# Performance work log

Hardware: AMD Instinct MI355X
Metric: run time of the kernel (lower is better)

Reference implementation:

```python
import jax, jax.numpy as jnp
import numpy as np

N, IN_DIM, HID, HEADS, OUT = 4096, 512, 256, 2, 40
LN_EPS = 1e-5


def setup_inputs() -> dict:
    key = jax.random.key(0)
    ks = jax.random.split(key, 12)
    s_in = 1.0 / np.sqrt(IN_DIM)
    s_o = 1.0 / np.sqrt(2 * HID)
    adj = jax.random.randint(ks[0], (HEADS, N, N), 0, 2).astype(jnp.float32)
    h = jax.random.normal(ks[1], (N, IN_DIM), dtype=jnp.float32)
    Wq = jax.random.uniform(ks[2], (HEADS, IN_DIM, HID), minval=-s_in, maxval=s_in)
    bq = jax.random.uniform(ks[3], (HEADS, HID), minval=-s_in, maxval=s_in)
    Wk = jax.random.uniform(ks[4], (HEADS, IN_DIM, HID), minval=-s_in, maxval=s_in)
    bk = jax.random.uniform(ks[5], (HEADS, HID), minval=-s_in, maxval=s_in)
    Wv = jax.random.uniform(ks[6], (HEADS, IN_DIM, HID), minval=-s_in, maxval=s_in)
    bv = jax.random.uniform(ks[7], (HEADS, HID), minval=-s_in, maxval=s_in)
    Wo = jax.random.uniform(ks[8], (2 * HID, IN_DIM), minval=-s_o, maxval=s_o)
    bo = jax.random.uniform(ks[9], (IN_DIM,), minval=-s_o, maxval=s_o)
    gamma = jnp.ones((IN_DIM,), jnp.float32)
    beta = jnp.zeros((IN_DIM,), jnp.float32)
    Wp = jax.random.uniform(ks[10], (IN_DIM, OUT), minval=-s_in, maxval=s_in)
    bp = jax.random.uniform(ks[11], (OUT,), minval=-s_in, maxval=s_in)
    return dict(adj=adj, h=h, Wq=Wq, bq=bq, Wk=Wk, bk=bk, Wv=Wv, bv=bv,
                Wo=Wo, bo=bo, gamma=gamma, beta=beta, Wp=Wp, bp=bp)


def reference(adj, h, Wq, bq, Wk, bk, Wv, bv, Wo, bo, gamma, beta, Wp, bp):
    # Per-head projections, vectorized over the head axis. [H, N, D]
    Q = jnp.einsum('ni,hid->hnd', h, Wq) + bq[:, None, :]
    K = jnp.einsum('ni,hid->hnd', h, Wk) + bk[:, None, :]
    V = jnp.einsum('ni,hid->hnd', h, Wv) + bv[:, None, :]
    # Dense QK^T, elementwise-multiplied (not -inf masked) by per-head adjacency.
    scores = jnp.einsum('hnd,hmd->hnm', Q, K) * adj          # [H, N, N]
    attn = jax.nn.softmax(scores, axis=-1)
    X = jnp.einsum('hnm,hmd->hnd', attn, V)                  # [H, N, D]
    # cat([X0, X1], dim=1) -> [N, H*D]
    X_final = jnp.transpose(X, (1, 0, 2)).reshape(N, HEADS * HID)
    z = X_final @ Wo + bo                                    # [N, IN_DIM]
    mu = jnp.mean(z, axis=-1, keepdims=True)
    var = jnp.var(z, axis=-1, keepdims=True)
    M = (z - mu) * jax.lax.rsqrt(var + LN_EPS) * gamma + beta
    return jax.nn.softmax(M @ Wp + bp, axis=1)               # [N, OUT]
```

## Files before the change

kernel.cpp:

```cpp
#include <hip/hip_runtime.h>
#include <hip/hip_bf16.h>

#define N_TOK 4096
#define D_IN  512
#define D_HID 256
#define N_OUT 40

typedef _Float16 half8 __attribute__((ext_vector_type(8)));
typedef _Float16 half4 __attribute__((ext_vector_type(4)));
typedef float    f32x4 __attribute__((ext_vector_type(4)));

__device__ __forceinline__ void async_copy16(const _Float16* g, _Float16* l) {
  __builtin_amdgcn_global_load_lds(
      (const __attribute__((address_space(1))) unsigned int*)(g),
      (__attribute__((address_space(3))) unsigned int*)(l), 16, 0, 0);
}

__device__ __forceinline__ void transpose_tile(const float* __restrict__ src, int in_ncols,
                                               _Float16* __restrict__ dst, int out_ncols,
                                               int i0, int d0, float* lds )
{
  int tid = threadIdx.x;
  int l15 = tid & 15, l4 = tid >> 4;
#pragma unroll
  for (int p = 0; p < 4; p++) {
    int ii = p * 16 + l4;
    float4 x = *(const float4*)(src + (size_t)(i0 + ii) * in_ncols + d0 + l15 * 4);
    lds[(l15 * 4 + 0) * 65 + ii] = x.x;
    lds[(l15 * 4 + 1) * 65 + ii] = x.y;
    lds[(l15 * 4 + 2) * 65 + ii] = x.z;
    lds[(l15 * 4 + 3) * 65 + ii] = x.w;
  }
  __syncthreads();
  int dd = tid >> 2, chunk = tid & 3;
  half8 o0, o1;
#pragma unroll
  for (int j = 0; j < 8; j++) o0[j] = (_Float16)lds[dd * 65 + chunk * 16 + j];
#pragma unroll
  for (int j = 0; j < 8; j++) o1[j] = (_Float16)lds[dd * 65 + chunk * 16 + 8 + j];
  *(half8*)(dst + (size_t)(d0 + dd) * out_ncols + i0 + chunk * 16) = o0;
  *(half8*)(dst + (size_t)(d0 + dd) * out_ncols + i0 + chunk * 16 + 8) = o1;
}

__global__ void prep_kernel(const float* __restrict__ h, const float* __restrict__ Wq,
                            const float* __restrict__ Wk, const float* __restrict__ Wv,
                            const float* __restrict__ Wo, const float* __restrict__ Wp,
                            _Float16* __restrict__ h16, _Float16* __restrict__ Wqt,
                            _Float16* __restrict__ Wkt, _Float16* __restrict__ Wvt,
                            _Float16* __restrict__ Wot, _Float16* __restrict__ Wpt)
{
  __shared__ float lds[64 * 65];
  int b = blockIdx.x, tid = threadIdx.x;
  if (b < 1024) {
    int base = b * 2048 + tid * 8;
    float4 x0 = *(const float4*)(h + base);
    float4 x1 = *(const float4*)(h + base + 4);
    half8 o;
    o[0]=(_Float16)x0.x; o[1]=(_Float16)x0.y; o[2]=(_Float16)x0.z; o[3]=(_Float16)x0.w;
    o[4]=(_Float16)x1.x; o[5]=(_Float16)x1.y; o[6]=(_Float16)x1.z; o[7]=(_Float16)x1.w;
    *(half8*)(h16 + base) = o;
  } else if (b < 1216) {
    int t = b - 1024;
    int mat = t >> 5;
    int m = mat >> 1, head = mat & 1;
    const float* W = (m==0 ? Wq : (m==1 ? Wk : Wv)) + head * (D_IN * D_HID);
    _Float16* Wt   = (m==0 ? Wqt : (m==1 ? Wkt : Wvt)) + head * (D_IN * D_HID);
    int tt = t & 31;
    int i0 = (tt >> 2) * 64, d0 = (tt & 3) * 64;
    transpose_tile(W, D_HID, Wt, D_IN, i0, d0, lds);
  } else if (b < 1280) {
    int t = b - 1216;
    int i0 = (t >> 3) * 64, d0 = (t & 7) * 64;
    transpose_tile(Wo, D_IN, Wot, D_IN, i0, d0, lds);
  } else {
    int blk = b - 1280;
    int idx = blk * 1024 + tid * 4;
    int j = idx >> 9, i = idx & 511;
    half4 o;
#pragma unroll
    for (int u = 0; u < 4; u++)
      o[u] = (j < N_OUT) ? (_Float16)Wp[(i + u) * N_OUT + j] : (_Float16)0.f;
    *(half4*)(Wpt + j * D_IN + i) = o;
  }
}

__global__ __launch_bounds__(256, 2) void proj_kernel(
    const _Float16* __restrict__ h16, const _Float16* __restrict__ W6 ,
    const _Float16* __restrict__ Wvt,
    const float* __restrict__ bq, const float* __restrict__ bk,
    const float* __restrict__ bv,
    _Float16* __restrict__ Q16, _Float16* __restrict__ K16,
    _Float16* __restrict__ VT16)
{
  __shared__ __align__(16) _Float16 Atile[128 * 64];
  __shared__ __align__(16) _Float16 Btile[128 * 64];

  int b = blockIdx.x;
  int tid = threadIdx.x, w = tid >> 6, lane = tid & 63, quad = lane >> 4, cL = lane & 15;
  int wr = w >> 1, wc = w & 1;

  const _Float16 *Asrc, *Bsrc;
  int isV;
  int m0 = 0, n0 = 0, head = 0, mh = 0;
  if (b < 256) {
    isV = 0;
    m0 = (b >> 3) * 128;
    int ct = b & 7;
    mh = ct >> 1;
    n0 = (ct & 1) * 128;
    Asrc = h16 + (size_t)m0 * D_IN;
    Bsrc = W6 + (size_t)(ct * 128) * D_IN;
  } else {
    isV = 1;
    int t = b - 256;
    head = t >> 6;
    int tt = t & 63;
    m0 = (tt >> 5) * 128;
    n0 = (tt & 31) * 128;
    Asrc = Wvt + (size_t)head * (D_HID * D_IN) + (size_t)m0 * D_IN;
    Bsrc = h16 + (size_t)n0 * D_IN;
  }

  const f32x4 z4 = {0.f, 0.f, 0.f, 0.f};
  f32x4 acc[4][4];
#pragma unroll
  for (int i = 0; i < 4; i++)
#pragma unroll
    for (int j = 0; j < 4; j++) acc[i][j] = z4;

  int r8 = lane >> 3, chs = (lane & 7) ^ r8;

  for (int kc = 0; kc < 8; kc++) {
    __syncthreads();
#pragma unroll
    for (int g = 0; g < 4; g++) {
      int row = (w * 4 + g) * 8 + r8;
      async_copy16(Asrc + (size_t)row * D_IN + kc * 64 + chs * 8, Atile + (w * 4 + g) * 512);
      async_copy16(Bsrc + (size_t)row * D_IN + kc * 64 + chs * 8, Btile + (w * 4 + g) * 512);
    }
    __syncthreads();
#pragma unroll
    for (int kk = 0; kk < 2; kk++) {
      int ch = ((kk * 4 + quad) ^ (cL & 7)) * 8;
      half8 a[4], bf[4];
#pragma unroll
      for (int mt = 0; mt < 4; mt++)
        a[mt] = *(const half8*)(Atile + (wr * 64 + mt * 16 + cL) * 64 + ch);
#pragma unroll
      for (int nt = 0; nt < 4; nt++)
        bf[nt] = *(const half8*)(Btile + (wc * 64 + nt * 16 + cL) * 64 + ch);
#pragma unroll
      for (int mt = 0; mt < 4; mt++)
#pragma unroll
        for (int nt = 0; nt < 4; nt++)
          acc[mt][nt] = __builtin_amdgcn_mfma_f32_16x16x32_f16(a[mt], bf[nt], acc[mt][nt], 0, 0, 0);
    }
  }

  if (!isV) {
    _Float16* Out = (mh < 2 ? Q16 + (size_t)mh * (N_TOK * D_HID)
                            : K16 + (size_t)(mh - 2) * (N_TOK * D_HID));
    const float* bias = (mh < 2 ? bq + mh * D_HID : bk + (mh - 2) * D_HID);
#pragma unroll
    for (int mt = 0; mt < 4; mt++) {
      int row = m0 + wr * 64 + mt * 16 + quad * 4;
#pragma unroll
      for (int nt = 0; nt < 4; nt++) {
        int colg = n0 + wc * 64 + nt * 16 + cL;
        float bb = bias[colg];
#pragma unroll
        for (int reg = 0; reg < 4; reg++)
          Out[(size_t)(row + reg) * D_HID + colg] = (_Float16)(acc[mt][nt][reg] + bb);
      }
    }
  } else {
    _Float16* VTh = VT16 + (size_t)head * (N_TOK * D_HID);
    const float* bvh = bv + head * D_HID;
#pragma unroll
    for (int mt = 0; mt < 4; mt++) {
      int d0r = m0 + wr * 64 + mt * 16 + quad * 4;
      float bvv[4];
#pragma unroll
      for (int reg = 0; reg < 4; reg++) bvv[reg] = bvh[d0r + reg];
#pragma unroll
      for (int nt = 0; nt < 4; nt++) {
        int tok = n0 + wc * 64 + nt * 16 + cL;
#pragma unroll
        for (int reg = 0; reg < 4; reg++)
          VTh[(size_t)(d0r + reg) * N_TOK + tok] = (_Float16)(acc[mt][nt][reg] + bvv[reg]);
      }
    }
  }
}

__global__ __launch_bounds__(256, 2) void attn_kernel(
    const float* __restrict__ adj, const _Float16* __restrict__ Q16,
    const _Float16* __restrict__ K16, const _Float16* __restrict__ VT16,
    _Float16* __restrict__ Opart, float* __restrict__ Mpart, float* __restrict__ Lpart)
{
  __shared__ __align__(16) _Float16 Ktile[64 * 256];
  __shared__ __align__(16) _Float16 VTtile[256 * 64];
  __shared__ __align__(16) _Float16 Pbuf[4 * 16 * 72];

  int b = blockIdx.x;
  int head = (b >> 2) & 1;
  int gs = b & 3;
  int q0 = (b >> 3) * 64;

  int tid = threadIdx.x;
  int w = tid >> 6, lane = tid & 63, quad = lane >> 4, cL = lane & 15;

  const _Float16* Qh = Q16 + head * (N_TOK * D_HID);
  const _Float16* Kh = K16 + head * (N_TOK * D_HID);
  const _Float16* Vh = VT16 + head * (N_TOK * D_HID);
  const float* adjh = adj + (size_t)head * N_TOK * N_TOK;

  int qrow = q0 + w * 16;
  int nstart = gs * 1024;
  const f32x4 z4 = {0.f, 0.f, 0.f, 0.f};

  half8 qf[8];
#pragma unroll
  for (int t = 0; t < 8; t++)
    qf[t] = *(const half8*)(Qh + (qrow + cL) * D_HID + t * 32 + quad * 8);

  f32x4 acc[16];
#pragma unroll
  for (int i = 0; i < 16; i++) acc[i] = z4;
  float m_i[4] = {-1e30f, -1e30f, -1e30f, -1e30f};
  float l_i[4] = {0.f, 0.f, 0.f, 0.f};

  _Float16* pb = Pbuf + w * (16 * 72);

  const float* adjR[4];
#pragma unroll
  for (int reg = 0; reg < 4; reg++)
    adjR[reg] = adjh + (size_t)(qrow + quad * 4 + reg) * N_TOK + nstart + cL;

  int l5 = lane >> 5, l31 = lane & 31;
  int l3 = lane >> 3, l7 = lane & 7;

  for (int it = 0; it < 16; ++it) {
    int n0 = nstart + it * 64;

    __syncthreads();

#pragma unroll
    for (int i = 0; i < 8; i++) {
      int g = w * 8 + i;
      int rK = 2 * g + l5;
      int cK = l31 ^ (rK & 7);
      async_copy16(Kh + (size_t)(n0 + rK) * D_HID + cK * 8, Ktile + g * 512);
      int rV = g * 8 + l3;
      int cV = l7 ^ (rV & 7);
      async_copy16(Vh + (size_t)rV * N_TOK + n0 + cV * 8, VTtile + g * 512);
    }
    float av[4][4];
#pragma unroll
    for (int reg = 0; reg < 4; reg++)
#pragma unroll
      for (int ct = 0; ct < 4; ct++)
        av[reg][ct] = __builtin_nontemporal_load(adjR[reg] + it * 64 + ct * 16);

    __syncthreads();

    f32x4 s[4];
#pragma unroll
    for (int ct = 0; ct < 4; ct++) s[ct] = z4;
#pragma unroll
    for (int t = 0; t < 8; t++) {
#pragma unroll
      for (int ct = 0; ct < 4; ct++) {
        int rK = ct * 16 + cL;
        int ck = (t * 4 + quad) ^ (rK & 7);
        half8 kf = *(const half8*)(Ktile + rK * 256 + ck * 8);
        s[ct] = __builtin_amdgcn_mfma_f32_16x16x32_f16(qf[t], kf, s[ct], 0, 0, 0);
      }
    }

    float alpha[4];
#pragma unroll
    for (int reg = 0; reg < 4; reg++) {
#pragma unroll
      for (int ct = 0; ct < 4; ct++) s[ct][reg] *= av[reg][ct];
      float mx = fmaxf(fmaxf(s[0][reg], s[1][reg]), fmaxf(s[2][reg], s[3][reg]));
#pragma unroll
      for (int msk = 1; msk < 16; msk <<= 1) mx = fmaxf(mx, __shfl_xor(mx, msk, 16));
      float mnew = fmaxf(m_i[reg], mx);
      alpha[reg] = __expf(m_i[reg] - mnew);
      m_i[reg] = mnew;
      float rs = 0.f;
#pragma unroll
      for (int ct = 0; ct < 4; ct++) {
        float p = __expf(s[ct][reg] - mnew);
        s[ct][reg] = p;
        rs += p;
      }
#pragma unroll
      for (int msk = 1; msk < 16; msk <<= 1) rs += __shfl_xor(rs, msk, 16);
      l_i[reg] = l_i[reg] * alpha[reg] + rs;
    }

#pragma unroll
    for (int reg = 0; reg < 4; reg++)
#pragma unroll
      for (int ct = 0; ct < 4; ct++)
        pb[(quad * 4 + reg) * 72 + ct * 16 + cL] = (_Float16)s[ct][reg];

#pragma unroll
    for (int dt = 0; dt < 16; dt++)
#pragma unroll
      for (int reg = 0; reg < 4; reg++)
        acc[dt][reg] *= alpha[reg];

    half8 pf0 = *(const half8*)(pb + cL * 72 + quad * 8);
    half8 pf1 = *(const half8*)(pb + cL * 72 + 32 + quad * 8);
#pragma unroll
    for (int dt = 0; dt < 16; dt++) {
      int rV = dt * 16 + cL;
      int c0 = (quad) ^ (rV & 7);
      int c1 = (4 + quad) ^ (rV & 7);
      half8 v0 = *(const half8*)(VTtile + rV * 64 + c0 * 8);
      half8 v1 = *(const half8*)(VTtile + rV * 64 + c1 * 8);
      acc[dt] = __builtin_amdgcn_mfma_f32_16x16x32_f16(pf0, v0, acc[dt], 0, 0, 0);
      acc[dt] = __builtin_amdgcn_mfma_f32_16x16x32_f16(pf1, v1, acc[dt], 0, 0, 0);
    }
  }

  int prow = (head * 4 + gs) * N_TOK + qrow + quad * 4;
#pragma unroll
  for (int reg = 0; reg < 4; reg++) {
    int row = prow + reg;
#pragma unroll
    for (int dt = 0; dt < 16; dt++)
      Opart[(size_t)row * D_HID + dt * 16 + cL] = (_Float16)acc[dt][reg];
    if (cL == 0) { Mpart[row] = m_i[reg]; Lpart[row] = l_i[reg]; }
  }
}

__global__ void merge_kernel(const _Float16* __restrict__ Opart,
                             const float* __restrict__ Mpart,
                             const float* __restrict__ Lpart,
                             _Float16* __restrict__ Xf)
{
  int t = blockIdx.x * 256 + threadIdx.x;
  int dg = (t & 63) << 2;
  int n = (t >> 6) & (N_TOK - 1);
  int head = t >> 18;
  int idx[4];
  float m[4], l[4];
  float mm = -1e30f;
#pragma unroll
  for (int s = 0; s < 4; s++) {
    idx[s] = (head * 4 + s) * N_TOK + n;
    m[s] = Mpart[idx[s]];
    l[s] = Lpart[idx[s]];
    mm = fmaxf(mm, m[s]);
  }
  float f[4], L = 0.f;
#pragma unroll
  for (int s = 0; s < 4; s++) { f[s] = __expf(m[s] - mm); L += f[s] * l[s]; }
  float rl = 1.0f / L;
  float o[4] = {0.f, 0.f, 0.f, 0.f};
#pragma unroll
  for (int s = 0; s < 4; s++) {
    half4 os = *(const half4*)(Opart + (size_t)idx[s] * D_HID + dg);
#pragma unroll
    for (int u = 0; u < 4; u++) o[u] += (float)os[u] * f[s];
  }
  half4 res;
#pragma unroll
  for (int u = 0; u < 4; u++) res[u] = (_Float16)(o[u] * rl);
  *(half4*)(Xf + (size_t)n * D_IN + head * D_HID + dg) = res;
}

__global__ __launch_bounds__(256, 1) void final_kernel(
    const _Float16* __restrict__ Xf, const _Float16* __restrict__ Wot,
    const _Float16* __restrict__ Wpt, const float* __restrict__ bo,
    const float* __restrict__ gamma, const float* __restrict__ beta,
    const float* __restrict__ bp, float* __restrict__ out)
{
  __shared__ __align__(16) _Float16 Btile[512 * 64];
  __shared__ __align__(16) _Float16 Mlds[16 * 520];
  __shared__ float outs[16 * 48];
  __shared__ float lnsum[4][16], lnsq[4][16];
  __shared__ float smx[16], srl[16];

  int rowbase = blockIdx.x * 16;
  int tid = threadIdx.x, w = tid >> 6, lane = tid & 63, quad = lane >> 4, cL = lane & 15;
  const f32x4 z4 = {0.f, 0.f, 0.f, 0.f};

  half8 af[16];
#pragma unroll
  for (int t = 0; t < 16; t++)
    af[t] = *(const half8*)(Xf + (rowbase + cL) * D_IN + t * 32 + quad * 8);

  f32x4 acc[8];
#pragma unroll
  for (int i = 0; i < 8; i++) acc[i] = z4;

  int r8 = lane >> 3, chs = (lane & 7) ^ r8;

  for (int kc = 0; kc < 8; kc++) {
    __syncthreads();
#pragma unroll
    for (int g = 0; g < 16; g++) {
      int row = (w * 16 + g) * 8 + r8;
      async_copy16(Wot + (size_t)row * D_IN + kc * 64 + chs * 8, Btile + (w * 16 + g) * 512);
    }
    __syncthreads();
#pragma unroll
    for (int kk = 0; kk < 2; kk++) {
      int ch = ((kk * 4 + quad) ^ (cL & 7)) * 8;
      half8 a = af[kc * 2 + kk];
      half8 bf[8];
#pragma unroll
      for (int nt = 0; nt < 8; nt++)
        bf[nt] = *(const half8*)(Btile + (w * 128 + nt * 16 + cL) * 64 + ch);
#pragma unroll
      for (int nt = 0; nt < 8; nt++)
        acc[nt] = __builtin_amdgcn_mfma_f32_16x16x32_f16(a, bf[nt], acc[nt], 0, 0, 0);
    }
  }

  float sum[4] = {0, 0, 0, 0}, sq[4] = {0, 0, 0, 0};
#pragma unroll
  for (int nt = 0; nt < 8; nt++) {
    int col = w * 128 + nt * 16 + cL;
    float bb = bo[col];
#pragma unroll
    for (int reg = 0; reg < 4; reg++) {
      float z = acc[nt][reg] + bb;
      acc[nt][reg] = z;
      sum[reg] += z;
      sq[reg] += z * z;
    }
  }
#pragma unroll
  for (int reg = 0; reg < 4; reg++) {
#pragma unroll
    for (int msk = 1; msk < 16; msk <<= 1) {
      sum[reg] += __shfl_xor(sum[reg], msk, 16);
      sq[reg]  += __shfl_xor(sq[reg], msk, 16);
    }
  }
  if (cL == 0) {
#pragma unroll
    for (int reg = 0; reg < 4; reg++) {
      lnsum[w][quad * 4 + reg] = sum[reg];
      lnsq[w][quad * 4 + reg]  = sq[reg];
    }
  }
  __syncthreads();
  float mean[4], rstd[4];
#pragma unroll
  for (int reg = 0; reg < 4; reg++) {
    int row = quad * 4 + reg;
    float s  = lnsum[0][row] + lnsum[1][row] + lnsum[2][row] + lnsum[3][row];
    float s2 = lnsq[0][row]  + lnsq[1][row]  + lnsq[2][row]  + lnsq[3][row];
    float mu = s * (1.0f / 512.0f);
    float var = s2 * (1.0f / 512.0f) - mu * mu;
    mean[reg] = mu;
    rstd[reg] = rsqrtf(var + 1e-5f);
  }
#pragma unroll
  for (int nt = 0; nt < 8; nt++) {
    int col = w * 128 + nt * 16 + cL;
    float g = gamma[col], be = beta[col];
#pragma unroll
    for (int reg = 0; reg < 4; reg++) {
      float mval = (acc[nt][reg] - mean[reg]) * rstd[reg] * g + be;
      Mlds[(quad * 4 + reg) * 520 + col] = (_Float16)mval;
    }
  }
  __syncthreads();
  if (w < 3) {
    int jt = w;
    f32x4 a2 = z4;
#pragma unroll
    for (int t = 0; t < 16; t++) {
      half8 am = *(const half8*)(Mlds + cL * 520 + t * 32 + quad * 8);
      half8 bm = *(const half8*)(Wpt + (jt * 16 + cL) * D_IN + t * 32 + quad * 8);
      a2 = __builtin_amdgcn_mfma_f32_16x16x32_f16(am, bm, a2, 0, 0, 0);
    }
    int col = jt * 16 + cL;
    float bpv = (col < N_OUT) ? bp[col] : 0.0f;
#pragma unroll
    for (int reg = 0; reg < 4; reg++)
      outs[(quad * 4 + reg) * 48 + col] = a2[reg] + bpv;
  }
  __syncthreads();
  if (tid < 16) {
    int row = tid;
    float mx = -1e30f;
    for (int j = 0; j < N_OUT; j++) mx = fmaxf(mx, outs[row * 48 + j]);
    float ssum = 0.f;
    for (int j = 0; j < N_OUT; j++) ssum += __expf(outs[row * 48 + j] - mx);
    smx[row] = mx;
    srl[row] = 1.0f / ssum;
  }
  __syncthreads();
#pragma unroll
  for (int i = 0; i < 3; i++) {
    int lin = tid + 256 * i;
    if (lin < 16 * N_OUT) {
      int row = lin / N_OUT, col = lin % N_OUT;
      out[(size_t)(rowbase + row) * N_OUT + col] =
          __expf(outs[row * 48 + col] - smx[row]) * srl[row];
    }
  }
}

#define OFF_WOT   0u
#define OFF_WPT   524288u
#define OFF_Q16   573440u
#define OFF_K16   4767744u
#define OFF_VT16  8962048u
#define OFF_MP    13156352u
#define OFF_LP    13287424u
#define OFF_XF    13418496u
#define OFF_OP    17612800u
#define OFF_H16   17612800u
#define OFF_WQT   21807104u
#define OFF_WKT   22331392u
#define OFF_WVT   22855680u

extern "C" void kernel_launch(void* const* d_in, const int* in_sizes, int n_in,
                              void* d_out, int out_size, void* d_ws, size_t ws_size,
                              hipStream_t stream)
{
  const float* adj   = (const float*)d_in[0];
  const float* h     = (const float*)d_in[1];
  const float* Wq    = (const float*)d_in[2];
  const float* bq    = (const float*)d_in[3];
  const float* Wk    = (const float*)d_in[4];
  const float* bk    = (const float*)d_in[5];
  const float* Wv    = (const float*)d_in[6];
  const float* bv    = (const float*)d_in[7];
  const float* Wo    = (const float*)d_in[8];
  const float* bo    = (const float*)d_in[9];
  const float* gamma = (const float*)d_in[10];
  const float* beta  = (const float*)d_in[11];
  const float* Wp    = (const float*)d_in[12];
  const float* bp    = (const float*)d_in[13];
  float* out = (float*)d_out;
  char* ws = (char*)d_ws;

  _Float16* h16   = (_Float16*)(ws + OFF_H16);
  _Float16* Wqt   = (_Float16*)(ws + OFF_WQT);
  _Float16* Wkt   = (_Float16*)(ws + OFF_WKT);
  _Float16* Wvt   = (_Float16*)(ws + OFF_WVT);
  _Float16* Wot   = (_Float16*)(ws + OFF_WOT);
  _Float16* Wpt   = (_Float16*)(ws + OFF_WPT);
  _Float16* Q16   = (_Float16*)(ws + OFF_Q16);
  _Float16* K16   = (_Float16*)(ws + OFF_K16);
  _Float16* VT16  = (_Float16*)(ws + OFF_VT16);
  _Float16* Opart = (_Float16*)(ws + OFF_OP);
  float*    Mpart = (float*)(ws + OFF_MP);
  float*    Lpart = (float*)(ws + OFF_LP);
  _Float16* Xf    = (_Float16*)(ws + OFF_XF);

  prep_kernel<<<1304, 256, 0, stream>>>(h, Wq, Wk, Wv, Wo, Wp,
                                        h16, Wqt, Wkt, Wvt, Wot, Wpt);
  proj_kernel<<<384, 256, 0, stream>>>(h16, Wqt, Wvt, bq, bk, bv,
                                       Q16, K16, VT16);
  attn_kernel<<<512, 256, 0, stream>>>(adj, Q16, K16, VT16, Opart, Mpart, Lpart);
  merge_kernel<<<2048, 256, 0, stream>>>(Opart, Mpart, Lpart, Xf);
  final_kernel<<<256, 256, 0, stream>>>(Xf, Wot, Wpt, bo, gamma, beta, bp, out);
}
```

Measured before the change: 299.9 us.

## Double-buffer K/V tiles with 32-key steps and prefetch next tile during compute

The attention loop now uses 32-key tiles in two LDS buffers. The next K/V tile and its adjacency values are issued asynchronously before computing on the current tile, with one barrier per step instead of two. It also skips rescaling the accumulator when no row max changed in the wave. LDS use stays about the same, but the step count doubles and each step does half the MFMA work, so per-iteration overheads (shuffles, barriers) rise relative to compute.

```diff
diff --git a/kernel.cpp b/kernel.cpp
--- a/kernel.cpp
+++ b/kernel.cpp
@@ -198,9 +198,9 @@
     const _Float16* __restrict__ K16, const _Float16* __restrict__ VT16,
     _Float16* __restrict__ Opart, float* __restrict__ Mpart, float* __restrict__ Lpart)
 {
-  __shared__ __align__(16) _Float16 Ktile[64 * 256];
-  __shared__ __align__(16) _Float16 VTtile[256 * 64];
-  __shared__ __align__(16) _Float16 Pbuf[4 * 16 * 72];
+  __shared__ __align__(16) _Float16 Kt[2][32 * 256];
+  __shared__ __align__(16) _Float16 Vt[2][256 * 32];
+  __shared__ __align__(16) _Float16 Pbuf[4 * 16 * 40];
 
   int b = blockIdx.x;
   int head = (b >> 2) & 1;
@@ -230,7 +230,7 @@
   float m_i[4] = {-1e30f, -1e30f, -1e30f, -1e30f};
   float l_i[4] = {0.f, 0.f, 0.f, 0.f};
 
-  _Float16* pb = Pbuf + w * (16 * 72);
+  _Float16* pb = Pbuf + w * (16 * 40);
 
   const float* adjR[4];
 #pragma unroll
@@ -238,42 +238,53 @@
     adjR[reg] = adjh + (size_t)(qrow + quad * 4 + reg) * N_TOK + nstart + cL;
 
   int l5 = lane >> 5, l31 = lane & 31;
-  int l3 = lane >> 3, l7 = lane & 7;
-
-  for (int it = 0; it < 16; ++it) {
-    int n0 = nstart + it * 64;
-
-    __syncthreads();
-
-#pragma unroll
-    for (int i = 0; i < 8; i++) {
-      int g = w * 8 + i;
+  int l2 = lane >> 2, l3m = lane & 3;
+
+  auto stageK = [&](int it, _Float16* dst) {
+    int n0 = nstart + it * 32;
+#pragma unroll
+    for (int i = 0; i < 4; i++) {
+      int g = w * 4 + i;
       int rK = 2 * g + l5;
       int cK = l31 ^ (rK & 7);
-      async_copy16(Kh + (size_t)(n0 + rK) * D_HID + cK * 8, Ktile + g * 512);
-      int rV = g * 8 + l3;
-      int cV = l7 ^ (rV & 7);
-      async_copy16(Vh + (size_t)rV * N_TOK + n0 + cV * 8, VTtile + g * 512);
-    }
-    float av[4][4];
+      async_copy16(Kh + (size_t)(n0 + rK) * D_HID + cK * 8, dst + g * 512);
+    }
+  };
+  auto stageV = [&](int it, _Float16* dst) {
+    int n0 = nstart + it * 32;
+#pragma unroll
+    for (int i = 0; i < 4; i++) {
+      int g = w * 4 + i;
+      int rV = g * 16 + l2;
+      int cV = l3m ^ ((rV >> 1) & 3);
+      async_copy16(Vh + (size_t)rV * N_TOK + n0 + cV * 8, dst + g * 512);
+    }
+  };
+  auto loadAdj = [&](int it, float (&av)[4][2]) {
 #pragma unroll
     for (int reg = 0; reg < 4; reg++)
 #pragma unroll
-      for (int ct = 0; ct < 4; ct++)
-        av[reg][ct] = __builtin_nontemporal_load(adjR[reg] + it * 64 + ct * 16);
-
-    __syncthreads();
-
-    f32x4 s[4];
-#pragma unroll
-    for (int ct = 0; ct < 4; ct++) s[ct] = z4;
+      for (int ct = 0; ct < 2; ct++)
+        av[reg][ct] = __builtin_nontemporal_load(adjR[reg] + it * 32 + ct * 16);
+  };
+
+  auto body = [&](int it, const _Float16* KC, const _Float16* VC,
+                  _Float16* KN, _Float16* VN,
+                  float (&avC)[4][2], float (&avN)[4][2]) {
+    if (it + 1 < 32) {
+      stageK(it + 1, KN);
+      stageV(it + 1, VN);
+      loadAdj(it + 1, avN);
+    }
+
+    f32x4 s[2] = {z4, z4};
 #pragma unroll
     for (int t = 0; t < 8; t++) {
 #pragma unroll
-      for (int ct = 0; ct < 4; ct++) {
+      for (int ct = 0; ct < 2; ct++) {
         int rK = ct * 16 + cL;
         int ck = (t * 4 + quad) ^ (rK & 7);
-        half8 kf = *(const half8*)(Ktile + rK * 256 + ck * 8);
+        half8 kf = *(const half8*)(KC + rK * 256 + ck * 8);
         s[ct] = __builtin_amdgcn_mfma_f32_16x16x32_f16(qf[t], kf, s[ct], 0, 0, 0);
       }
     }
@@ -281,21 +292,19 @@
     float alpha[4];
 #pragma unroll
     for (int reg = 0; reg < 4; reg++) {
-#pragma unroll
-      for (int ct = 0; ct < 4; ct++) s[ct][reg] *= av[reg][ct];
-      float mx = fmaxf(fmaxf(s[0][reg], s[1][reg]), fmaxf(s[2][reg], s[3][reg]));
+      s[0][reg] *= avC[reg][0];
+      s[1][reg] *= avC[reg][1];
+      float mx = fmaxf(s[0][reg], s[1][reg]);
 #pragma unroll
       for (int msk = 1; msk < 16; msk <<= 1) mx = fmaxf(mx, __shfl_xor(mx, msk, 16));
       float mnew = fmaxf(m_i[reg], mx);
       alpha[reg] = __expf(m_i[reg] - mnew);
       m_i[reg] = mnew;
-      float rs = 0.f;
-#pragma unroll
-      for (int ct = 0; ct < 4; ct++) {
-        float p = __expf(s[ct][reg] - mnew);
-        s[ct][reg] = p;
-        rs += p;
-      }
+      float p0 = __expf(s[0][reg] - mnew);
+      float p1 = __expf(s[1][reg] - mnew);
+      s[0][reg] = p0;
+      s[1][reg] = p1;
+      float rs = p0 + p1;
 #pragma unroll
       for (int msk = 1; msk < 16; msk <<= 1) rs += __shfl_xor(rs, msk, 16);
       l_i[reg] = l_i[reg] * alpha[reg] + rs;
@@ -304,27 +313,38 @@
 #pragma unroll
     for (int reg = 0; reg < 4; reg++)
 #pragma unroll
-      for (int ct = 0; ct < 4; ct++)
-        pb[(quad * 4 + reg) * 72 + ct * 16 + cL] = (_Float16)s[ct][reg];
-
-#pragma unroll
-    for (int dt = 0; dt < 16; dt++)
-#pragma unroll
-      for (int reg = 0; reg < 4; reg++)
-        acc[dt][reg] *= alpha[reg];
-
-    half8 pf0 = *(const half8*)(pb + cL * 72 + quad * 8);
-    half8 pf1 = *(const half8*)(pb + cL * 72 + 32 + quad * 8);
+      for (int ct = 0; ct < 2; ct++)
+        pb[(quad * 4 + reg) * 40 + ct * 16 + cL] = (_Float16)s[ct][reg];
+
+    if (__any(alpha[0] * alpha[1] * alpha[2] * alpha[3] != 1.0f)) {
+#pragma unroll
+      for (int dt = 0; dt < 16; dt++)
+#pragma unroll
+        for (int reg = 0; reg < 4; reg++)
+          acc[dt][reg] *= alpha[reg];
+    }
+
+    half8 pf = *(const half8*)(pb + cL * 40 + quad * 8);
 #pragma unroll
     for (int dt = 0; dt < 16; dt++) {
       int rV = dt * 16 + cL;
-      int c0 = (quad) ^ (rV & 7);
-      int c1 = (4 + quad) ^ (rV & 7);
-      half8 v0 = *(const half8*)(VTtile + rV * 64 + c0 * 8);
-      half8 v1 = *(const half8*)(VTtile + rV * 64 + c1 * 8);
-      acc[dt] = __builtin_amdgcn_mfma_f32_16x16x32_f16(pf0, v0, acc[dt], 0, 0, 0);
-      acc[dt] = __builtin_amdgcn_mfma_f32_16x16x32_f16(pf1, v1, acc[dt], 0, 0, 0);
-    }
+      int cr = quad ^ ((rV >> 1) & 3);
+      half8 v = *(const half8*)(VC + rV * 32 + cr * 8);
+      acc[dt] = __builtin_amdgcn_mfma_f32_16x16x32_f16(pf, v, acc[dt], 0, 0, 0);
+    }
+
+    __syncthreads();
+  };
+
+  stageK(0, Kt[0]);
+  stageV(0, Vt[0]);
+  float avA[4][2], avB[4][2];
+  loadAdj(0, avA);
+  __syncthreads();
+
+  for (int itp = 0; itp < 16; ++itp) {
+    body(2 * itp,     Kt[0], Vt[0], Kt[1], Vt[1], avA, avB);
+    body(2 * itp + 1, Kt[1], Vt[1], Kt[0], Vt[0], avB, avA);
   }
 
   int prow = (head * 4 + gs) * N_TOK + qrow + quad * 4;
```

After: 308.6 us. +2.9%, slower.

## Double-buffer K/adjacency and projection tiles, read V from global, skip unit rescale

Applied to the files above, without the earlier changes.

The projection GEMM now double-buffers its LDS A/B tiles, so the next k-chunk's async copy is issued before computing on the current one. The attention kernel double-buffers the K tile and prefetches the next iteration's adjacency values into registers. It drops the V^T LDS staging and has each wave load V fragments straight from global memory. The accumulator rescale is skipped when every alpha in the wave equals one. The aim is to hide load latency and remove one barrier per iteration, at the cost of duplicated per-wave V reads from global/L2 and more live registers.

```diff
diff --git a/kernel.cpp b/kernel.cpp
--- a/kernel.cpp
+++ b/kernel.cpp
@@ -92,8 +92,8 @@
     _Float16* __restrict__ Q16, _Float16* __restrict__ K16,
     _Float16* __restrict__ VT16)
 {
-  __shared__ __align__(16) _Float16 Atile[128 * 64];
-  __shared__ __align__(16) _Float16 Btile[128 * 64];
+  __shared__ __align__(16) _Float16 Atile[2][128 * 64];
+  __shared__ __align__(16) _Float16 Btile[2][128 * 64];
 
   int b = blockIdx.x;
   int tid = threadIdx.x, w = tid >> 6, lane = tid & 63, quad = lane >> 4, cL = lane & 15;
@@ -130,31 +130,38 @@
 
   int r8 = lane >> 3, chs = (lane & 7) ^ r8;
 
-  for (int kc = 0; kc < 8; kc++) {
-    __syncthreads();
+  auto stage = [&](int kc, int pb) {
 #pragma unroll
     for (int g = 0; g < 4; g++) {
       int row = (w * 4 + g) * 8 + r8;
-      async_copy16(Asrc + (size_t)row * D_IN + kc * 64 + chs * 8, Atile + (w * 4 + g) * 512);
-      async_copy16(Bsrc + (size_t)row * D_IN + kc * 64 + chs * 8, Btile + (w * 4 + g) * 512);
-    }
-    __syncthreads();
+      async_copy16(Asrc + (size_t)row * D_IN + kc * 64 + chs * 8, Atile[pb] + (w * 4 + g) * 512);
+      async_copy16(Bsrc + (size_t)row * D_IN + kc * 64 + chs * 8, Btile[pb] + (w * 4 + g) * 512);
+    }
+  };
+
+  stage(0, 0);
+  __syncthreads();
+
+  for (int kc = 0; kc < 8; kc++) {
+    int cur = kc & 1;
+    if (kc + 1 < 8) stage(kc + 1, cur ^ 1);
 #pragma unroll
     for (int kk = 0; kk < 2; kk++) {
       int ch = ((kk * 4 + quad) ^ (cL & 7)) * 8;
       half8 a[4], bf[4];
 #pragma unroll
       for (int mt = 0; mt < 4; mt++)
-        a[mt] = *(const half8*)(Atile + (wr * 64 + mt * 16 + cL) * 64 + ch);
+        a[mt] = *(const half8*)(Atile[cur] + (wr * 64 + mt * 16 + cL) * 64 + ch);
 #pragma unroll
       for (int nt = 0; nt < 4; nt++)
-        bf[nt] = *(const half8*)(Btile + (wc * 64 + nt * 16 + cL) * 64 + ch);
+        bf[nt] = *(const half8*)(Btile[cur] + (wc * 64 + nt * 16 + cL) * 64 + ch);
 #pragma unroll
       for (int mt = 0; mt < 4; mt++)
 #pragma unroll
         for (int nt = 0; nt < 4; nt++)
           acc[mt][nt] = __builtin_amdgcn_mfma_f32_16x16x32_f16(a[mt], bf[nt], acc[mt][nt], 0, 0, 0);
     }
+    __syncthreads();
   }
 
   if (!isV) {
@@ -198,8 +205,7 @@
     const _Float16* __restrict__ K16, const _Float16* __restrict__ VT16,
     _Float16* __restrict__ Opart, float* __restrict__ Mpart, float* __restrict__ Lpart)
 {
-  __shared__ __align__(16) _Float16 Ktile[64 * 256];
-  __shared__ __align__(16) _Float16 VTtile[256 * 64];
+  __shared__ __align__(16) _Float16 Kt[2][64 * 256];
   __shared__ __align__(16) _Float16 Pbuf[4 * 16 * 72];
 
   int b = blockIdx.x;
@@ -238,31 +244,32 @@
     adjR[reg] = adjh + (size_t)(qrow + quad * 4 + reg) * N_TOK + nstart + cL;
 
   int l5 = lane >> 5, l31 = lane & 31;
-  int l3 = lane >> 3, l7 = lane & 7;
-
-  for (int it = 0; it < 16; ++it) {
+
+  auto stageK = [&](int it, _Float16* dst) {
     int n0 = nstart + it * 64;
-
-    __syncthreads();
-
 #pragma unroll
     for (int i = 0; i < 8; i++) {
       int g = w * 8 + i;
       int rK = 2 * g + l5;
       int cK = l31 ^ (rK & 7);
-      async_copy16(Kh + (size_t)(n0 + rK) * D_HID + cK * 8, Ktile + g * 512);
-      int rV = g * 8 + l3;
-      int cV = l7 ^ (rV & 7);
-      async_copy16(Vh + (size_t)rV * N_TOK + n0 + cV * 8, VTtile + g * 512);
-    }
-    float av[4][4];
+      async_copy16(Kh + (size_t)(n0 + rK) * D_HID + cK * 8, dst + g * 512);
+    }
+  };
+  auto loadAdj = [&](int it, float (&av)[4][4]) {
 #pragma unroll
     for (int reg = 0; reg < 4; reg++)
 #pragma unroll
       for (int ct = 0; ct < 4; ct++)
         av[reg][ct] = __builtin_nontemporal_load(adjR[reg] + it * 64 + ct * 16);
-
-    __syncthreads();
+  };
+
+  auto body = [&](int it, const _Float16* KC, _Float16* KN,
+                  float (&avC)[4][4], float (&avN)[4][4]) {
+    int n0 = nstart + it * 64;
+    if (it + 1 < 16) {
+      stageK(it + 1, KN);
+      loadAdj(it + 1, avN);
+    }
 
     f32x4 s[4];
 #pragma unroll
@@ -273,7 +280,7 @@
       for (int ct = 0; ct < 4; ct++) {
         int rK = ct * 16 + cL;
         int ck = (t * 4 + quad) ^ (rK & 7);
-        half8 kf = *(const half8*)(Ktile + rK * 256 + ck * 8);
+        half8 kf = *(const half8*)(KC + rK * 256 + ck * 8);
         s[ct] = __builtin_amdgcn_mfma_f32_16x16x32_f16(qf[t], kf, s[ct], 0, 0, 0);
       }
     }
@@ -282,7 +289,7 @@
 #pragma unroll
     for (int reg = 0; reg < 4; reg++) {
 #pragma unroll
-      for (int ct = 0; ct < 4; ct++) s[ct][reg] *= av[reg][ct];
+      for (int ct = 0; ct < 4; ct++) s[ct][reg] *= avC[reg][ct];
       float mx = fmaxf(fmaxf(s[0][reg], s[1][reg]), fmaxf(s[2][reg], s[3][reg]));
 #pragma unroll
       for (int msk = 1; msk < 16; msk <<= 1) mx = fmaxf(mx, __shfl_xor(mx, msk, 16));
@@ -307,24 +314,37 @@
       for (int ct = 0; ct < 4; ct++)
         pb[(quad * 4 + reg) * 72 + ct * 16 + cL] = (_Float16)s[ct][reg];
 
-#pragma unroll
-    for (int dt = 0; dt < 16; dt++)
-#pragma unroll
-      for (int reg = 0; reg < 4; reg++)
-        acc[dt][reg] *= alpha[reg];
+    if (__any(alpha[0] * alpha[1] * alpha[2] * alpha[3] != 1.0f)) {
+#pragma unroll
+      for (int dt = 0; dt < 16; dt++)
+#pragma unroll
+        for (int reg = 0; reg < 4; reg++)
+          acc[dt][reg] *= alpha[reg];
+    }
 
     half8 pf0 = *(const half8*)(pb + cL * 72 + quad * 8);
     half8 pf1 = *(const half8*)(pb + cL * 72 + 32 + quad * 8);
 #pragma unroll
     for (int dt = 0; dt < 16; dt++) {
       int rV = dt * 16 + cL;
-      int c0 = (quad) ^ (rV & 7);
-      int c1 = (4 + quad) ^ (rV & 7);
-      half8 v0 = *(const half8*)(VTtile + rV * 64 + c0 * 8);
-      half8 v1 = *(const half8*)(VTtile + rV * 64 + c1 * 8);
+      const _Float16* vp = Vh + (size_t)rV * N_TOK + n0 + quad * 8;
+      half8 v0 = *(const half8*)(vp);
+      half8 v1 = *(const half8*)(vp + 32);
       acc[dt] = __builtin_amdgcn_mfma_f32_16x16x32_f16(pf0, v0, acc[dt], 0, 0, 0);
       acc[dt] = __builtin_amdgcn_mfma_f32_16x16x32_f16(pf1, v1, acc[dt], 0, 0, 0);
     }
+
+    __syncthreads();
+  };
+
+  stageK(0, Kt[0]);
+  float avA[4][4], avB[4][4];
+  loadAdj(0, avA);
+  __syncthreads();
+
+  for (int itp = 0; itp < 8; ++itp) {
+    body(2 * itp,     Kt[0], Kt[1], avA, avB);
+    body(2 * itp + 1, Kt[1], Kt[0], avB, avA);
   }
 
   int prow = (head * 4 + gs) * N_TOK + qrow + quad * 4;
```

Result: slower. 389.6 us (+29.9%).
